# Optimization experiments

Measured on AMD Instinct MI355X. Metric: run time of the kernel, lower is better.

Reference implementation:

```python
import jax, jax.numpy as jnp
import numpy as np


def _ternarize(p, delta, w):
    # {-w, 0, +w} via threshold mask, matching TrainableTernarize.forward
    return jnp.where(p > delta, w, jnp.where(p < -delta, -w, jnp.zeros_like(p)))


def _ternary_para(p, w):
    # TrainableTernaryPara.forward: delta = 0.05 * max|p|
    delta = 0.05 * jnp.max(jnp.abs(p))
    return _ternarize(p, delta, w)


def _init_scale(p):
    # w init: mean(|p|[|p| > 0.7 * mean|p|])
    a = jnp.abs(p)
    mask = (a > 0.7 * jnp.mean(a)).astype(p.dtype)
    return jnp.sum(a * mask) / jnp.sum(mask)


def setup_inputs() -> dict:
    key = jax.random.key(0)
    k1, k2, k3 = jax.random.split(key, 3)
    B, S, D_IN, D_OUT = 4, 2048, 4096, 4096
    x = jax.random.normal(k1, (B, S, D_IN), dtype=jnp.float32)
    bound = 1.0 / np.sqrt(D_IN)  # nn.Linear default init range
    W = jax.random.uniform(k2, (D_OUT, D_IN), minval=-bound, maxval=bound, dtype=jnp.float32)
    b = jax.random.uniform(k3, (D_OUT,), minval=-bound, maxval=bound, dtype=jnp.float32)
    w_scale = _init_scale(W)
    b_scale = _init_scale(b)
    return {"x": x, "W": W, "w_scale": w_scale, "b": b, "b_scale": b_scale}


def reference(x, W, w_scale, b, b_scale):
    Wt = _ternary_para(W, w_scale)   # [D_OUT, D_IN] in {-w,0,+w}
    bt = _ternary_para(b, b_scale)   # [D_OUT]
    # F.linear(x, Wt, bt) = x @ Wt.T + bt
    return jnp.einsum('bsi,oi->bso', x, Wt) + bt
```

## Files before the change

### kernel.cpp

```cpp
#include <hip/hip_runtime.h>

typedef int v4i __attribute__((ext_vector_type(4)));

#define BM 256
#define BN 256
#define BKB 64
#define NRING 4

#define GLOAD_LDS(gptr, lptr)                                                         \
  __builtin_amdgcn_global_load_lds(                                                   \
      (const __attribute__((address_space(1))) unsigned int*)(gptr),                  \
      (__attribute__((address_space(3))) unsigned int*)(lptr), 16, 0, 0)


__global__ void absmax2_kernel(const float4* __restrict__ W4, long nW4,
                               const float4* __restrict__ b4, int nb4,
                               unsigned* __restrict__ mx) {
  __shared__ float sm[4];
  float m = 0.f;
  const bool isB = (blockIdx.x == gridDim.x - 1);
  if (!isB) {
    const long stride = (long)(gridDim.x - 1) * blockDim.x;
    for (long i = blockIdx.x * (long)blockDim.x + threadIdx.x; i < nW4; i += stride) {
      float4 v = W4[i];
      m = fmaxf(m, fmaxf(fmaxf(fabsf(v.x), fabsf(v.y)), fmaxf(fabsf(v.z), fabsf(v.w))));
    }
  } else {
    for (int i = threadIdx.x; i < nb4; i += blockDim.x) {
      float4 v = b4[i];
      m = fmaxf(m, fmaxf(fmaxf(fabsf(v.x), fabsf(v.y)), fmaxf(fabsf(v.z), fabsf(v.w))));
    }
  }
  for (int off = 32; off > 0; off >>= 1)
    m = fmaxf(m, __shfl_down(m, off));
  if ((threadIdx.x & 63) == 0) sm[threadIdx.x >> 6] = m;
  __syncthreads();
  if (threadIdx.x == 0) {
    m = fmaxf(fmaxf(sm[0], sm[1]), fmaxf(sm[2], sm[3]));
    atomicMax(mx + (isB ? 1 : 0), __float_as_uint(m));
  }
}

__global__ void xquant_kernel(const float4* __restrict__ X4,
                              signed char* __restrict__ Q,
                              float* __restrict__ sx, int K) {
  __shared__ float sm[4];
  const int row = blockIdx.x;
  const int tid = threadIdx.x;
  const float4* xr = X4 + (size_t)row * (K / 4);
  float4 v[4];
  float m = 0.f;
#pragma unroll
  for (int i = 0; i < 4; ++i) {
    v[i] = xr[tid + i * 256];
    m = fmaxf(m, fmaxf(fmaxf(fabsf(v[i].x), fabsf(v[i].y)),
                       fmaxf(fabsf(v[i].z), fabsf(v[i].w))));
  }
  for (int off = 32; off > 0; off >>= 1) m = fmaxf(m, __shfl_down(m, off));
  if ((tid & 63) == 0) sm[tid >> 6] = m;
  __syncthreads();
  const float total = fmaxf(fmaxf(sm[0], sm[1]), fmaxf(sm[2], sm[3]));
  const float inv = 127.f / total;
  int* qw = (int*)(Q + (size_t)row * K);
#pragma unroll
  for (int i = 0; i < 4; ++i) {
    const float* f = (const float*)&v[i];
    int b[4];
#pragma unroll
    for (int j = 0; j < 4; ++j) {
      float r = rintf(f[j] * inv);
      r = fmaxf(-127.f, fminf(127.f, r));
      b[j] = ((int)r) & 255;
    }
    qw[tid + i * 256] = b[0] | (b[1] << 8) | (b[2] << 16) | (b[3] << 24);
  }
  if (tid == 0) sx[row] = total * (1.f / 127.f);
}

__global__ void prep_w_kernel(const float4* __restrict__ W4, long nW4,
                              const float4* __restrict__ b4, int nb4,
                              const unsigned* __restrict__ mx,
                              const float* __restrict__ bscale,
                              int* __restrict__ Twi, float4* __restrict__ bt) {
  if (blockIdx.x == gridDim.x - 1) {
    const float delta = 0.05f * __uint_as_float(mx[1]);
    const float s = *bscale;
    for (int i = threadIdx.x; i < nb4; i += blockDim.x) {
      float4 v = b4[i];
      float4 o;
      o.x = v.x > delta ? s : (v.x < -delta ? -s : 0.f);
      o.y = v.y > delta ? s : (v.y < -delta ? -s : 0.f);
      o.z = v.z > delta ? s : (v.z < -delta ? -s : 0.f);
      o.w = v.w > delta ? s : (v.w < -delta ? -s : 0.f);
      bt[i] = o;
    }
    return;
  }
  const float delta = 0.05f * __uint_as_float(mx[0]);
  const long stride = (long)(gridDim.x - 1) * blockDim.x;
  for (long i = blockIdx.x * (long)blockDim.x + threadIdx.x; i < nW4; i += stride) {
    float4 w = W4[i];
    int b0 = w.x > delta ? 1 : (w.x < -delta ? 0xFF : 0);
    int b1 = w.y > delta ? 1 : (w.y < -delta ? 0xFF : 0);
    int b2 = w.z > delta ? 1 : (w.z < -delta ? 0xFF : 0);
    int b3 = w.w > delta ? 1 : (w.w < -delta ? 0xFF : 0);
    Twi[i] = b0 | (b1 << 8) | (b2 << 16) | (b3 << 24);
  }
}

__global__ __launch_bounds__(512, 2) void gemm_tern_i8(
    const signed char* __restrict__ A,
    const signed char* __restrict__ B,
    const float* __restrict__ sx,
    const float* __restrict__ bt,
    const float* __restrict__ wsc,
    float* __restrict__ C,
    int M, int N, int K) {
  __shared__ __align__(16) signed char lds[NRING][2][BM * BKB];

  const int tid = threadIdx.x;
  const int wave = tid >> 6;
  const int lane = tid & 63;
  const int wm = wave >> 2, wn = wave & 3;
  const int quad = lane >> 4;
  const int l16 = lane & 15;

  const int bm0 = blockIdx.y * BM;
  const int bn0 = blockIdx.x * BN;

  const signed char* gA[2];
  const signed char* gB[2];
#pragma unroll
  for (int j = 0; j < 2; ++j) {
    const int idx = j * 512 + tid;
    const int row = idx >> 2;
    const int gch = (idx & 3) ^ ((idx >> 3) & 3);
    gA[j] = A + (size_t)(bm0 + row) * K + gch * 16;
    gB[j] = B + (size_t)(bn0 + row) * K + gch * 16;
  }
  const int ldsbase = wave * 64 * 16;

#define STAGE(slot)                                  \
  do {                                               \
    signed char* la = &lds[slot][0][ldsbase];        \
    signed char* lb = &lds[slot][1][ldsbase];        \
    GLOAD_LDS(gA[0], la);                            \
    GLOAD_LDS(gA[1], la + 8192);                     \
    GLOAD_LDS(gB[0], lb);                            \
    GLOAD_LDS(gB[1], lb + 8192);                     \
    gA[0] += BKB; gA[1] += BKB;                      \
    gB[0] += BKB; gB[1] += BKB;                      \
  } while (0)

  const int kchunk = quad ^ ((l16 >> 1) & 3);
  const int aoff = (wm * 128 + l16) * BKB + kchunk * 16;
  const int boff = (wn * 64 + l16) * BKB + kchunk * 16;

  v4i acc[8][4] = {};

  STAGE(0);
  STAGE(1);
  STAGE(2);
  asm volatile("s_waitcnt vmcnt(8)" ::: "memory");
  asm volatile("s_barrier" ::: "memory");

  const int NT = K / BKB;
  for (int t = 0; t < NT; ++t) {
    if (t + 3 < NT) STAGE((t + 3) & 3);
    const int slot = t & 3;
    const v4i* fA = (const v4i*)&lds[slot][0][aoff];
    const v4i* fB = (const v4i*)&lds[slot][1][boff];
    v4i af[8], bf[4];
#pragma unroll
    for (int i = 0; i < 8; ++i) af[i] = fA[i * 64];
#pragma unroll
    for (int i = 0; i < 4; ++i) bf[i] = fB[i * 64];
    __builtin_amdgcn_s_setprio(1);
#pragma unroll
    for (int mt = 0; mt < 8; ++mt)
#pragma unroll
      for (int nt = 0; nt < 4; ++nt)
        acc[mt][nt] = __builtin_amdgcn_mfma_i32_16x16x64_i8(
            af[mt], bf[nt], acc[mt][nt], 0, 0, 0);
    __builtin_amdgcn_s_setprio(0);
    asm volatile("s_waitcnt vmcnt(8)" ::: "memory");
    asm volatile("s_barrier" ::: "memory");
  }
#undef STAGE

  const float ws = *wsc;
#pragma unroll
  for (int mt = 0; mt < 8; ++mt) {
    const int row = bm0 + wm * 128 + mt * 16 + quad * 4;
    float sc[4];
#pragma unroll
    for (int r = 0; r < 4; ++r) sc[r] = ws * sx[row + r];
#pragma unroll
    for (int nt = 0; nt < 4; ++nt) {
      const int col = bn0 + wn * 64 + nt * 16 + l16;
      const float bias = bt[col];
#pragma unroll
      for (int r = 0; r < 4; ++r)
        C[(size_t)(row + r) * N + col] = sc[r] * (float)acc[mt][nt][r] + bias;
    }
  }
}


extern "C" void kernel_launch(void* const* d_in, const int* in_sizes, int n_in,
                              void* d_out, int out_size, void* d_ws, size_t ws_size,
                              hipStream_t stream) {
  const float* x = (const float*)d_in[0];
  const float* W = (const float*)d_in[1];
  const float* w_scale = (const float*)d_in[2];
  const float* b = (const float*)d_in[3];
  const float* b_scale = (const float*)d_in[4];
  float* out = (float*)d_out;

  const int K = 4096;
  const int N = in_sizes[3];
  const int M = in_sizes[0] / K;

  char* ws = (char*)d_ws;
  signed char* xb = (signed char*)ws;
  signed char* Tw = (signed char*)(ws + (size_t)M * K);
  float* bt = (float*)(ws + (size_t)M * K + (size_t)N * K);
  float* sx = bt + N;
  unsigned* mx = (unsigned*)(sx + M);

  hipMemsetAsync(mx, 0, 8, stream);

  const long nW4 = (long)N * K / 4;
  const int nb4 = N / 4;

  absmax2_kernel<<<1025, 256, 0, stream>>>((const float4*)W, nW4,
                                           (const float4*)b, nb4, mx);

  xquant_kernel<<<M, 256, 0, stream>>>((const float4*)x, xb, sx, K);

  prep_w_kernel<<<8193, 256, 0, stream>>>((const float4*)W, nW4,
                                          (const float4*)b, nb4, mx, b_scale,
                                          (int*)Tw, (float4*)bt);

  dim3 gg(N / BN, M / BM);
  gemm_tern_i8<<<gg, 512, 0, stream>>>(xb, Tw, sx, bt, w_scale, out, M, N, K);
}
```

Before: 409.2 us.

## Fuse prep kernels, remap GEMM tiles per XCD, interleave loads with MFMA quarters

Merges the x quantization and W/b absmax passes into one launch and lowers the prep_w grid size. The GEMM grid becomes 1D, with a mapping that gives each XCD a contiguous band of M tiles so the L2 can reuse A rows. The main loop is split into four MFMA quarter-blocks, with LDS fragment loads and A/B global-to-LDS prefetches placed between them behind barriers. This aims to overlap memory traffic with compute, at the cost of more barriers per K step. The tile mapping hardcodes 8 XCDs and M/BM = 32.

```diff
diff --git a/kernel.cpp b/kernel.cpp
--- a/kernel.cpp
+++ b/kernel.cpp
@@ -13,68 +13,63 @@
       (__attribute__((address_space(3))) unsigned int*)(lptr), 16, 0, 0)
 
 
-__global__ void absmax2_kernel(const float4* __restrict__ W4, long nW4,
-                               const float4* __restrict__ b4, int nb4,
-                               unsigned* __restrict__ mx) {
+__device__ __forceinline__ float max4abs(float4 v) {
+  return fmaxf(fmaxf(fabsf(v.x), fabsf(v.y)), fmaxf(fabsf(v.z), fabsf(v.w)));
+}
+
+__device__ __forceinline__ int packq4(float4 v, float inv) {
+  int b0 = ((int)fminf(127.f, fmaxf(-127.f, rintf(v.x * inv)))) & 255;
+  int b1 = ((int)fminf(127.f, fmaxf(-127.f, rintf(v.y * inv)))) & 255;
+  int b2 = ((int)fminf(127.f, fmaxf(-127.f, rintf(v.z * inv)))) & 255;
+  int b3 = ((int)fminf(127.f, fmaxf(-127.f, rintf(v.w * inv)))) & 255;
+  return b0 | (b1 << 8) | (b2 << 16) | (b3 << 24);
+}
+
+__global__ void prep1_kernel(const float4* __restrict__ X4,
+                             signed char* __restrict__ Q,
+                             float* __restrict__ sx, int K, int nrows,
+                             const float4* __restrict__ W4, long nW4,
+                             const float4* __restrict__ b4, int nb4,
+                             unsigned* __restrict__ mx) {
   __shared__ float sm[4];
+  const int tid = threadIdx.x;
+  const int bid = blockIdx.x;
+
+  if (bid < nrows) {
+    const float4* xr = X4 + (size_t)bid * (K / 4);
+    float4 v0 = xr[tid], v1 = xr[tid + 256], v2 = xr[tid + 512], v3 = xr[tid + 768];
+    float m = fmaxf(fmaxf(max4abs(v0), max4abs(v1)), fmaxf(max4abs(v2), max4abs(v3)));
+    for (int off = 32; off > 0; off >>= 1) m = fmaxf(m, __shfl_down(m, off));
+    if ((tid & 63) == 0) sm[tid >> 6] = m;
+    __syncthreads();
+    const float total = fmaxf(fmaxf(sm[0], sm[1]), fmaxf(sm[2], sm[3]));
+    const float inv = 127.f / total;
+    int* qw = (int*)(Q + (size_t)bid * K);
+    qw[tid]       = packq4(v0, inv);
+    qw[tid + 256] = packq4(v1, inv);
+    qw[tid + 512] = packq4(v2, inv);
+    qw[tid + 768] = packq4(v3, inv);
+    if (tid == 0) sx[bid] = total * (1.f / 127.f);
+    return;
+  }
+
   float m = 0.f;
-  const bool isB = (blockIdx.x == gridDim.x - 1);
+  const bool isB = (bid == gridDim.x - 1);
   if (!isB) {
-    const long stride = (long)(gridDim.x - 1) * blockDim.x;
-    for (long i = blockIdx.x * (long)blockDim.x + threadIdx.x; i < nW4; i += stride) {
-      float4 v = W4[i];
-      m = fmaxf(m, fmaxf(fmaxf(fabsf(v.x), fabsf(v.y)), fmaxf(fabsf(v.z), fabsf(v.w))));
-    }
+    const long wb = bid - nrows;
+    const long stride = 1024L * blockDim.x;
+    for (long i = wb * blockDim.x + tid; i < nW4; i += stride)
+      m = fmaxf(m, max4abs(W4[i]));
   } else {
-    for (int i = threadIdx.x; i < nb4; i += blockDim.x) {
-      float4 v = b4[i];
-      m = fmaxf(m, fmaxf(fmaxf(fabsf(v.x), fabsf(v.y)), fmaxf(fabsf(v.z), fabsf(v.w))));
-    }
-  }
-  for (int off = 32; off > 0; off >>= 1)
-    m = fmaxf(m, __shfl_down(m, off));
-  if ((threadIdx.x & 63) == 0) sm[threadIdx.x >> 6] = m;
-  __syncthreads();
-  if (threadIdx.x == 0) {
-    m = fmaxf(fmaxf(sm[0], sm[1]), fmaxf(sm[2], sm[3]));
-    atomicMax(mx + (isB ? 1 : 0), __float_as_uint(m));
-  }
-}
-
-__global__ void xquant_kernel(const float4* __restrict__ X4,
-                              signed char* __restrict__ Q,
-                              float* __restrict__ sx, int K) {
-  __shared__ float sm[4];
-  const int row = blockIdx.x;
-  const int tid = threadIdx.x;
-  const float4* xr = X4 + (size_t)row * (K / 4);
-  float4 v[4];
-  float m = 0.f;
-#pragma unroll
-  for (int i = 0; i < 4; ++i) {
-    v[i] = xr[tid + i * 256];
-    m = fmaxf(m, fmaxf(fmaxf(fabsf(v[i].x), fabsf(v[i].y)),
-                       fmaxf(fabsf(v[i].z), fabsf(v[i].w))));
+    for (int i = tid; i < nb4; i += blockDim.x) m = fmaxf(m, max4abs(b4[i]));
   }
   for (int off = 32; off > 0; off >>= 1) m = fmaxf(m, __shfl_down(m, off));
   if ((tid & 63) == 0) sm[tid >> 6] = m;
   __syncthreads();
-  const float total = fmaxf(fmaxf(sm[0], sm[1]), fmaxf(sm[2], sm[3]));
-  const float inv = 127.f / total;
-  int* qw = (int*)(Q + (size_t)row * K);
-#pragma unroll
-  for (int i = 0; i < 4; ++i) {
-    const float* f = (const float*)&v[i];
-    int b[4];
-#pragma unroll
-    for (int j = 0; j < 4; ++j) {
-      float r = rintf(f[j] * inv);
-      r = fmaxf(-127.f, fminf(127.f, r));
-      b[j] = ((int)r) & 255;
-    }
-    qw[tid + i * 256] = b[0] | (b[1] << 8) | (b[2] << 16) | (b[3] << 24);
-  }
-  if (tid == 0) sx[row] = total * (1.f / 127.f);
+  if (tid == 0) {
+    m = fmaxf(fmaxf(sm[0], sm[1]), fmaxf(sm[2], sm[3]));
+    atomicMax(mx + (isB ? 1 : 0), __float_as_uint(m));
+  }
 }
 
 __global__ void prep_w_kernel(const float4* __restrict__ W4, long nW4,
@@ -125,8 +120,13 @@
   const int quad = lane >> 4;
   const int l16 = lane & 15;
 
-  const int bm0 = blockIdx.y * BM;
-  const int bn0 = blockIdx.x * BN;
+  const unsigned orig = blockIdx.x;
+  const unsigned xcd = orig & 7;
+  const unsigned r8 = orig >> 3;
+  const int by = (int)(xcd * 4 + (r8 & 3));
+  const int bx = (int)(r8 >> 2);
+  const int bm0 = by * BM;
+  const int bn0 = bx * BN;
 
   const signed char* gA[2];
   const signed char* gB[2];
@@ -140,17 +140,25 @@
   }
   const int ldsbase = wave * 64 * 16;
 
-#define STAGE(slot)                                  \
+#define STAGE_A(slot)                                \
   do {                                               \
     signed char* la = &lds[slot][0][ldsbase];        \
-    signed char* lb = &lds[slot][1][ldsbase];        \
     GLOAD_LDS(gA[0], la);                            \
     GLOAD_LDS(gA[1], la + 8192);                     \
+    gA[0] += BKB; gA[1] += BKB;                      \
+  } while (0)
+#define STAGE_B(slot)                                \
+  do {                                               \
+    signed char* lb = &lds[slot][1][ldsbase];        \
     GLOAD_LDS(gB[0], lb);                            \
     GLOAD_LDS(gB[1], lb + 8192);                     \
-    gA[0] += BKB; gA[1] += BKB;                      \
     gB[0] += BKB; gB[1] += BKB;                      \
   } while (0)
+
+#define BAR()  do { __builtin_amdgcn_sched_barrier(0); __builtin_amdgcn_s_barrier(); \
+                    __builtin_amdgcn_sched_barrier(0); } while (0)
+#define WAITLGKM() do { asm volatile("s_waitcnt lgkmcnt(0)" ::: "memory");           \
+                        __builtin_amdgcn_sched_barrier(0); } while (0)
 
   const int kchunk = quad ^ ((l16 >> 1) & 3);
   const int aoff = (wm * 128 + l16) * BKB + kchunk * 16;
@@ -158,35 +166,75 @@
 
   v4i acc[8][4] = {};
 
-  STAGE(0);
-  STAGE(1);
-  STAGE(2);
+  STAGE_A(0); STAGE_B(0);
+  STAGE_A(1); STAGE_B(1);
+  STAGE_A(2); STAGE_B(2);
   asm volatile("s_waitcnt vmcnt(8)" ::: "memory");
-  asm volatile("s_barrier" ::: "memory");
+  BAR();
 
   const int NT = K / BKB;
   for (int t = 0; t < NT; ++t) {
-    if (t + 3 < NT) STAGE((t + 3) & 3);
     const int slot = t & 3;
     const v4i* fA = (const v4i*)&lds[slot][0][aoff];
     const v4i* fB = (const v4i*)&lds[slot][1][boff];
+    const bool pf = (t + 3 < NT);
+    const int pslot = (t + 3) & 3;
     v4i af[8], bf[4];
-#pragma unroll
-    for (int i = 0; i < 8; ++i) af[i] = fA[i * 64];
-#pragma unroll
-    for (int i = 0; i < 4; ++i) bf[i] = fB[i * 64];
-    __builtin_amdgcn_s_setprio(1);
-#pragma unroll
-    for (int mt = 0; mt < 8; ++mt)
-#pragma unroll
-      for (int nt = 0; nt < 4; ++nt)
-        acc[mt][nt] = __builtin_amdgcn_mfma_i32_16x16x64_i8(
-            af[mt], bf[nt], acc[mt][nt], 0, 0, 0);
-    __builtin_amdgcn_s_setprio(0);
+
+    af[0] = fA[0]; af[1] = fA[64]; af[2] = fA[128]; af[3] = fA[192];
+    bf[0] = fB[0]; bf[1] = fB[64];
+    if (pf) STAGE_A(pslot);
+    BAR();
+    WAITLGKM();
+    __builtin_amdgcn_s_setprio(1);
+#pragma unroll
+    for (int mt = 0; mt < 4; ++mt)
+#pragma unroll
+      for (int nt = 0; nt < 2; ++nt)
+        acc[mt][nt] = __builtin_amdgcn_mfma_i32_16x16x64_i8(af[mt], bf[nt], acc[mt][nt], 0, 0, 0);
+    __builtin_amdgcn_s_setprio(0);
+    BAR();
+
+    bf[2] = fB[128]; bf[3] = fB[192];
+    if (pf) STAGE_B(pslot);
+    BAR();
+    WAITLGKM();
+    __builtin_amdgcn_s_setprio(1);
+#pragma unroll
+    for (int mt = 0; mt < 4; ++mt)
+#pragma unroll
+      for (int nt = 2; nt < 4; ++nt)
+        acc[mt][nt] = __builtin_amdgcn_mfma_i32_16x16x64_i8(af[mt], bf[nt], acc[mt][nt], 0, 0, 0);
+    __builtin_amdgcn_s_setprio(0);
+    BAR();
+
+    af[4] = fA[256]; af[5] = fA[320]; af[6] = fA[384]; af[7] = fA[448];
+    BAR();
+    WAITLGKM();
+    __builtin_amdgcn_s_setprio(1);
+#pragma unroll
+    for (int mt = 4; mt < 8; ++mt)
+#pragma unroll
+      for (int nt = 2; nt < 4; ++nt)
+        acc[mt][nt] = __builtin_amdgcn_mfma_i32_16x16x64_i8(af[mt], bf[nt], acc[mt][nt], 0, 0, 0);
+    __builtin_amdgcn_s_setprio(0);
+    BAR();
+
     asm volatile("s_waitcnt vmcnt(8)" ::: "memory");
-    asm volatile("s_barrier" ::: "memory");
-  }
-#undef STAGE
+    BAR();
+    __builtin_amdgcn_s_setprio(1);
+#pragma unroll
+    for (int mt = 4; mt < 8; ++mt)
+#pragma unroll
+      for (int nt = 0; nt < 2; ++nt)
+        acc[mt][nt] = __builtin_amdgcn_mfma_i32_16x16x64_i8(af[mt], bf[nt], acc[mt][nt], 0, 0, 0);
+    __builtin_amdgcn_s_setprio(0);
+    BAR();
+  }
+#undef STAGE_A
+#undef STAGE_B
+#undef BAR
+#undef WAITLGKM
 
   const float ws = *wsc;
 #pragma unroll
@@ -233,15 +281,14 @@
   const long nW4 = (long)N * K / 4;
   const int nb4 = N / 4;
 
-  absmax2_kernel<<<1025, 256, 0, stream>>>((const float4*)W, nW4,
-                                           (const float4*)b, nb4, mx);
-
-  xquant_kernel<<<M, 256, 0, stream>>>((const float4*)x, xb, sx, K);
-
-  prep_w_kernel<<<8193, 256, 0, stream>>>((const float4*)W, nW4,
+  prep1_kernel<<<M + 1024 + 1, 256, 0, stream>>>((const float4*)x, xb, sx, K, M,
+                                                 (const float4*)W, nW4,
+                                                 (const float4*)b, nb4, mx);
+
+  prep_w_kernel<<<2049, 256, 0, stream>>>((const float4*)W, nW4,
                                           (const float4*)b, nb4, mx, b_scale,
                                           (int*)Tw, (float4*)bt);
 
-  dim3 gg(N / BN, M / BM);
-  gemm_tern_i8<<<gg, 512, 0, stream>>>(xb, Tw, sx, bt, w_scale, out, M, N, K);
-}
+  const int nwg = (N / BN) * (M / BM);
+  gemm_tern_i8<<<nwg, 512, 0, stream>>>(xb, Tw, sx, bt, w_scale, out, M, N, K);
+}
```

Result: no change. 406.7 us (-0.6%).
